# Kernel optimization log

Hardware: AMD Instinct MI355X
Metric: run time of the kernel (lower is better)

Reference implementation:

```python
import jax, jax.numpy as jnp
import numpy as np

HID, OUT = 128, 16
N_USER, N_MOVIE, N_DIR = 200000, 100000, 20000
ALPHA, NUM_LAYERS = 0.01, 2


def _seg_mean(h_src, src, dst, n_dst):
    # copy_u + mean reduce: mean of incoming messages per dst node (0 if no in-edges)
    msg = h_src[src]                                   # [E, H] gather
    s = jax.ops.segment_sum(msg, dst, num_segments=n_dst)
    deg = jax.ops.segment_sum(jnp.ones((dst.shape[0],), h_src.dtype), dst, num_segments=n_dst)
    return s / jnp.maximum(deg, 1.0)[:, None]


def setup_inputs() -> dict:
    key = jax.random.key(0)
    ks = jax.random.split(key, 16)
    inp = {
        'x_user': jax.random.normal(ks[0], (N_USER, 128), jnp.float32),
        'x_movie': jax.random.normal(ks[1], (N_MOVIE, 128), jnp.float32),
        'x_director': jax.random.normal(ks[2], (N_DIR, 128), jnp.float32),
        'rates_src': jax.random.randint(ks[3], (600000,), 0, N_USER, jnp.int32),
        'rates_dst': jax.random.randint(ks[4], (600000,), 0, N_MOVIE, jnp.int32),
        'rby_src': jax.random.randint(ks[5], (600000,), 0, N_MOVIE, jnp.int32),
        'rby_dst': jax.random.randint(ks[6], (600000,), 0, N_USER, jnp.int32),
        'dir_src': jax.random.randint(ks[7], (100000,), 0, N_DIR, jnp.int32),
        'dir_dst': jax.random.randint(ks[8], (100000,), 0, N_MOVIE, jnp.int32),
        'dby_src': jax.random.randint(ks[9], (100000,), 0, N_MOVIE, jnp.int32),
        'dby_dst': jax.random.randint(ks[10], (100000,), 0, N_DIR, jnp.int32),
    }
    sc = 1.0 / np.sqrt(128.0)
    inp['W_user'] = jax.random.normal(ks[11], (HID, 128), jnp.float32) * sc
    inp['b_user'] = jnp.zeros((HID,), jnp.float32)
    inp['W_movie'] = jax.random.normal(ks[12], (HID, 128), jnp.float32) * sc
    inp['b_movie'] = jnp.zeros((HID,), jnp.float32)
    inp['W_director'] = jax.random.normal(ks[13], (HID, 128), jnp.float32) * sc
    inp['b_director'] = jnp.zeros((HID,), jnp.float32)
    inp['W_out'] = jax.random.normal(ks[14], (OUT, HID), jnp.float32) * (1.0 / np.sqrt(HID))
    inp['b_out'] = jnp.zeros((OUT,), jnp.float32)
    return inp


def reference(x_user, x_movie, x_director,
              W_user, b_user, W_movie, b_movie, W_director, b_director,
              W_out, b_out,
              rates_src, rates_dst, rby_src, rby_dst,
              dir_src, dir_dst, dby_src, dby_dst):
    # per-ntype input Linear + ReLU (num_lins = 1)
    h_u = jax.nn.relu(x_user @ W_user.T + b_user)
    h_m = jax.nn.relu(x_movie @ W_movie.T + b_movie)
    h_d = jax.nn.relu(x_director @ W_director.T + b_director)
    for _ in range(NUM_LAYERS):
        # per-etype segment-mean; cross_reducer='mean' over etypes targeting each ntype
        agg_m = 0.5 * (_seg_mean(h_u, rates_src, rates_dst, N_MOVIE)
                       + _seg_mean(h_d, dir_src, dir_dst, N_MOVIE))
        agg_u = _seg_mean(h_m, rby_src, rby_dst, N_USER)
        agg_d = _seg_mean(h_m, dby_src, dby_dst, N_DIR)
        h_u = ALPHA * h_u + agg_u
        h_m = ALPHA * h_m + agg_m
        h_d = ALPHA * h_d + agg_d
    return h_m @ W_out.T + b_out  # target ntype 'movie' logits [N_MOVIE, OUT]
```

## Files before the change

### kernel.cpp

```cpp
#include <hip/hip_runtime.h>

#define ALPHA 0.01f
#define BIN_SHIFT 10
#define SBIN 1024
#define CAPB 8192

typedef __attribute__((ext_vector_type(8))) short short8v;
typedef __attribute__((ext_vector_type(4))) float float4v;

__device__ __forceinline__ void bsplit(float x, unsigned short& hi, unsigned short& lo) {
  unsigned u = __float_as_uint(x);
  hi = (unsigned short)(u >> 16);
  float r = x - __uint_as_float(u & 0xFFFF0000u);
  lo = (unsigned short)(__float_as_uint(r) >> 16);
}

__device__ __forceinline__ void frag_from8(const float* v, short8v& hi, short8v& lo) {
#pragma unroll
  for (int e = 0; e < 8; ++e) {
    unsigned short h, l;
    bsplit(v[e], h, l);
    hi[e] = (short)h;
    lo[e] = (short)l;
  }
}

__global__ __launch_bounds__(256, 2) void fused_mfma3_kernel(
    const float* __restrict__ Xu, const float* __restrict__ Xm, const float* __restrict__ Xd,
    const float* __restrict__ Wu, const float* __restrict__ Wm, const float* __restrict__ Wd,
    const float* __restrict__ Bu, const float* __restrict__ Bm, const float* __restrict__ Bd,
    const float* __restrict__ Wo,
    float* __restrict__ Gu, float* __restrict__ Gm, float* __restrict__ Gd,
    int NU, int NM, int ND, int bu, int bm)
{
  __shared__ char smem[65536 + 10368] __attribute__((aligned(16)));
  unsigned short* Whi = (unsigned short*)smem;
  unsigned short* Wlo = (unsigned short*)(smem + 32768);
  unsigned short* WoHi = (unsigned short*)(smem + 65536);
  unsigned short* WoLo = (unsigned short*)(smem + 65536 + 4096);

  const float *X, *W, *B;
  float* G;
  int N, bid, nbk;
  if ((int)blockIdx.x < bu)            { X = Xu; W = Wu; B = Bu; G = Gu; N = NU; bid = blockIdx.x;            nbk = bu; }
  else if ((int)blockIdx.x < bu + bm)  { X = Xm; W = Wm; B = Bm; G = Gm; N = NM; bid = blockIdx.x - bu;       nbk = bm; }
  else                                 { X = Xd; W = Wd; B = Bd; G = Gd; N = ND; bid = blockIdx.x - bu - bm;  nbk = gridDim.x - bu - bm; }

  const int t = threadIdx.x;
  const int wave = t >> 6;
  const int lane = t & 63;
  const int s = lane & 15;
  const int q = lane >> 4;
  float* hbuf = (float*)(smem + 65536 + wave * 2176);

#pragma unroll
  for (int i = 0; i < 32; ++i) {
    int p = i * 256 + t;
    int row = p >> 6, c2 = p & 63;
    float w0 = W[row * 128 + c2 * 2];
    float w1 = W[row * 128 + c2 * 2 + 1];
    unsigned short h0, l0, h1, l1;
    bsplit(w0, h0, l0); bsplit(w1, h1, l1);
    int u32idx = row * 64 + ((((c2 * 4) ^ ((row & 7) << 4))) >> 2);
    ((unsigned*)Whi)[u32idx] = (unsigned)h0 | ((unsigned)h1 << 16);
    ((unsigned*)Wlo)[u32idx] = (unsigned)l0 | ((unsigned)l1 << 16);
  }
#pragma unroll
  for (int i = 0; i < 4; ++i) {
    int p = i * 256 + t;
    int row = p >> 6, c2 = p & 63;
    float w0 = Wo[row * 128 + c2 * 2];
    float w1 = Wo[row * 128 + c2 * 2 + 1];
    unsigned short h0, l0, h1, l1;
    bsplit(w0, h0, l0); bsplit(w1, h1, l1);
    int u32idx = row * 64 + ((((c2 * 4) ^ ((row & 7) << 4))) >> 2);
    ((unsigned*)WoHi)[u32idx] = (unsigned)h0 | ((unsigned)h1 << 16);
    ((unsigned*)WoLo)[u32idx] = (unsigned)l0 | ((unsigned)l1 << 16);
  }
  __syncthreads();

  short8v woh[4], wol[4];
  const int woswz = (s & 7) << 4;
#pragma unroll
  for (int ks = 0; ks < 4; ++ks) {
    int off = s * 256 + ((ks * 64 + q * 16) ^ woswz);
    woh[ks] = *(const short8v*)((char*)WoHi + off);
    wol[ks] = *(const short8v*)((char*)WoLo + off);
  }
  float bv[8];
#pragma unroll
  for (int nt = 0; nt < 8; ++nt) bv[nt] = B[nt * 16 + s];
  __syncthreads();

  const int nchunks = (N + 127) >> 7;
  const int bswz = (s & 7) << 4;

  for (int chunk = bid; chunk < nchunks; chunk += nbk) {
    const int rowbase = chunk * 128 + wave * 32;

    short8v ahi[2][4], alo[2][4];
#pragma unroll
    for (int mt = 0; mt < 2; ++mt) {
      int row = rowbase + mt * 16 + s;
      int crow = row < N ? row : (N - 1);
      const float* xr = X + (size_t)crow * 128;
#pragma unroll
      for (int ks = 0; ks < 4; ++ks) {
        float4 f0 = *(const float4*)(xr + ks * 32 + q * 8);
        float4 f1 = *(const float4*)(xr + ks * 32 + q * 8 + 4);
        float v[8] = {f0.x, f0.y, f0.z, f0.w, f1.x, f1.y, f1.z, f1.w};
        frag_from8(v, ahi[mt][ks], alo[mt][ks]);
      }
    }

    float4v acc[2][8];
#pragma unroll
    for (int mt = 0; mt < 2; ++mt)
#pragma unroll
      for (int nt = 0; nt < 8; ++nt) acc[mt][nt] = (float4v){0.f, 0.f, 0.f, 0.f};

#pragma unroll
    for (int ks = 0; ks < 4; ++ks) {
      short8v bh[8];
#pragma unroll
      for (int nt = 0; nt < 8; ++nt) {
        int c = nt * 16 + s;
        int off = c * 256 + ((ks * 64 + q * 16) ^ bswz);
        bh[nt] = *(const short8v*)((char*)Whi + off);
      }
#pragma unroll
      for (int nt = 0; nt < 8; ++nt) {
#pragma unroll
        for (int mt = 0; mt < 2; ++mt) {
          acc[mt][nt] = __builtin_amdgcn_mfma_f32_16x16x32_bf16(ahi[mt][ks], bh[nt], acc[mt][nt], 0, 0, 0);
          acc[mt][nt] = __builtin_amdgcn_mfma_f32_16x16x32_bf16(alo[mt][ks], bh[nt], acc[mt][nt], 0, 0, 0);
        }
      }
#pragma unroll
      for (int nt = 0; nt < 8; ++nt) {
        int c = nt * 16 + s;
        int off = c * 256 + ((ks * 64 + q * 16) ^ bswz);
        short8v bl = *(const short8v*)((char*)Wlo + off);
#pragma unroll
        for (int mt = 0; mt < 2; ++mt)
          acc[mt][nt] = __builtin_amdgcn_mfma_f32_16x16x32_bf16(ahi[mt][ks], bl, acc[mt][nt], 0, 0, 0);
      }
    }

#pragma unroll
    for (int mt = 0; mt < 2; ++mt) {
      float4v gacc = (float4v){0.f, 0.f, 0.f, 0.f};
#pragma unroll
      for (int ks = 0; ks < 4; ++ks) {
#pragma unroll
        for (int j = 0; j < 2; ++j) {
          int nt = 2 * ks + j;
          int cl = j * 16 + s;
#pragma unroll
          for (int e = 0; e < 4; ++e)
            hbuf[cl * 17 + q * 4 + e] = fmaxf(acc[mt][nt][e] + bv[nt], 0.f);
        }
        float hv[8];
#pragma unroll
        for (int e = 0; e < 8; ++e) hv[e] = hbuf[(q * 8 + e) * 17 + s];
        short8v hh, hl;
        frag_from8(hv, hh, hl);
        gacc = __builtin_amdgcn_mfma_f32_16x16x32_bf16(hh, woh[ks], gacc, 0, 0, 0);
        gacc = __builtin_amdgcn_mfma_f32_16x16x32_bf16(hl, woh[ks], gacc, 0, 0, 0);
        gacc = __builtin_amdgcn_mfma_f32_16x16x32_bf16(hh, wol[ks], gacc, 0, 0, 0);
      }
      int grow = rowbase + mt * 16 + 4 * q;
#pragma unroll
      for (int e = 0; e < 4; ++e)
        if (grow + e < N) G[(size_t)(grow + e) * 16 + s] = gacc[e];
    }
  }
}

__device__ __forceinline__ void edge_decode(
    int i, const int* ys, const int* yd, int Erby,
    const int* bs, const int* bd, int Edby,
    const int* rs, const int* rd, int Er,
    const int* ds, const int* dd,
    int NU, int& src, int& bucket, int& bin)
{
  if (i < Erby)            { src = ys[i]; bucket = yd[i];                 bin = bucket >> BIN_SHIFT; }
  else if (i < Erby + Edby){ int j = i - Erby; src = bs[j]; bucket = NU + bd[j]; bin = bucket >> BIN_SHIFT; }
  else if (i < Erby + Edby + Er) { int j = i - Erby - Edby; src = rs[j]; bucket = 2 * rd[j]; bin = 256 + (bucket >> BIN_SHIFT); }
  else                     { int j = i - Erby - Edby - Er; src = ds[j]; bucket = 2 * dd[j] + 1; bin = 256 + (bucket >> BIN_SHIFT); }
}

__global__ __launch_bounds__(256) void fill2_kernel(
    const int* __restrict__ ys, const int* __restrict__ yd, int Erby,
    const int* __restrict__ bs, const int* __restrict__ bd, int Edby,
    const int* __restrict__ rs, const int* __restrict__ rd, int Er,
    const int* __restrict__ ds, const int* __restrict__ dd, int Edir,
    int NU, int* __restrict__ cursor,
    unsigned* __restrict__ binnedA, unsigned* __restrict__ binnedB)
{
  __shared__ int h[512];
  __shared__ int base[512];
  const int E = Erby + Edby + Er + Edir;
  const int c0 = blockIdx.x * 4096;
  const int c1 = (c0 + 4096 < E) ? c0 + 4096 : E;
  h[threadIdx.x] = 0; h[threadIdx.x + 256] = 0;
  __syncthreads();
  for (int i = c0 + threadIdx.x; i < c1; i += 256) {
    int src, bucket, bin;
    edge_decode(i, ys, yd, Erby, bs, bd, Edby, rs, rd, Er, ds, dd, NU, src, bucket, bin);
    atomicAdd(&h[bin], 1);
  }
  __syncthreads();
#pragma unroll
  for (int k = threadIdx.x; k < 512; k += 256) {
    int c = h[k];
    base[k] = c ? atomicAdd(&cursor[k], c) : 0;
    h[k] = 0;
  }
  __syncthreads();
  for (int i = c0 + threadIdx.x; i < c1; i += 256) {
    int src, bucket, bin;
    edge_decode(i, ys, yd, Erby, bs, bd, Edby, rs, rd, Er, ds, dd, NU, src, bucket, bin);
    int r = atomicAdd(&h[bin], 1);
    int pos = base[bin] + r;
    if (pos < CAPB) {
      unsigned code = ((unsigned)src << BIN_SHIFT) | (unsigned)(bucket & (SBIN - 1));
      if (bin < 256) binnedA[(size_t)bin * CAPB + pos] = code;
      else           binnedB[(size_t)(bin - 256) * CAPB + pos] = code;
    }
  }
}

__global__ __launch_bounds__(256) void scatter2_kernel(
    const unsigned* __restrict__ binnedA, const unsigned* __restrict__ binnedB,
    const int* __restrict__ cursor, int nbinsA, int HA, int HB,
    int* __restrict__ bOffsA, int* __restrict__ bCntA,
    int* __restrict__ bOffsB, int* __restrict__ bCntB,
    int* __restrict__ ssrcA, int* __restrict__ ssrcB)
{
  __shared__ int cnt[SBIN];
  __shared__ int pref[SBIN];
  __shared__ int wsum[256];
  const int t = threadIdx.x;
  const bool isA = (int)blockIdx.x < nbinsA;
  const int b = isA ? (int)blockIdx.x : (int)blockIdx.x - nbinsA;
  const unsigned* win = (isA ? binnedA : binnedB) + (size_t)b * CAPB;
  int* bOffs = isA ? bOffsA : bOffsB;
  int* bCnt  = isA ? bCntA  : bCntB;
  int* ssrc  = isA ? ssrcA  : ssrcB;
  const int nbuckets = isA ? HA : HB;
  const size_t wbase = (size_t)b * CAPB;
  int n = cursor[isA ? b : 256 + b];
  if (n > CAPB) n = CAPB;

#pragma unroll
  for (int k = t; k < SBIN; k += 256) cnt[k] = 0;
  __syncthreads();
  for (int i = t; i < n; i += 256)
    atomicAdd(&cnt[win[i] & (SBIN - 1)], 1);
  __syncthreads();
  int c0 = cnt[4 * t], c1 = cnt[4 * t + 1], c2 = cnt[4 * t + 2], c3 = cnt[4 * t + 3];
  int s = c0 + c1 + c2 + c3;
  wsum[t] = s;
  __syncthreads();
  for (int d = 1; d < 256; d <<= 1) {
    int add = (t >= d) ? wsum[t - d] : 0;
    __syncthreads();
    wsum[t] += add;
    __syncthreads();
  }
  int base = wsum[t] - s;
  pref[4 * t]     = base;
  pref[4 * t + 1] = base + c0;
  pref[4 * t + 2] = base + c0 + c1;
  pref[4 * t + 3] = base + c0 + c1 + c2;
  __syncthreads();
  const int gb = b << BIN_SHIFT;
#pragma unroll
  for (int k = t; k < SBIN; k += 256) {
    int bucket = gb + k;
    if (bucket < nbuckets) { bOffs[bucket] = (int)(wbase + pref[k]); bCnt[bucket] = cnt[k]; }
  }
  __syncthreads();
#pragma unroll
  for (int k = t; k < SBIN; k += 256) cnt[k] = pref[k];
  __syncthreads();
  for (int i = t; i < n; i += 256) {
    unsigned code = win[i];
    int local = code & (SBIN - 1);
    int r = atomicAdd(&cnt[local], 1);
    ssrc[wbase + r] = (int)(code >> BIN_SHIFT);
  }
}

__global__ __launch_bounds__(256) void gather_pay2_kernel(
    const float* __restrict__ g_m, const float* __restrict__ g_u,
    const float* __restrict__ g_d,
    const int* __restrict__ bOffsA, const int* __restrict__ bCntA,
    const int* __restrict__ ssrcA,
    float* __restrict__ pay_u, float* __restrict__ pay_d, int NU, int ND)
{
  int tid = blockIdx.x * 256 + threadIdx.x;
  int node = tid >> 4, o = tid & 15;
  if (node >= NU + ND) return;
  int start = bOffsA[node], cnt = bCntA[node];
  float sum = 0.f;
  for (int j = 0; j < cnt; ++j) {
    int s = ssrcA[start + j];
    sum += g_m[(size_t)s * 16 + o];
  }
  float mean = 0.5f * sum / fmaxf((float)cnt, 1.f);
  if (node < NU)
    pay_u[(size_t)node * 16 + o] = ALPHA * g_u[(size_t)node * 16 + o] + mean;
  else {
    int nn = node - NU;
    pay_d[(size_t)nn * 16 + o] = ALPHA * g_d[(size_t)nn * 16 + o] + mean;
  }
}

__global__ __launch_bounds__(256) void final_kernel(
    const float* __restrict__ gm, const float* __restrict__ pay_u,
    const float* __restrict__ pay_d,
    const int* __restrict__ bOffs, const int* __restrict__ bCnt,
    const int* __restrict__ ssrc,
    const float* __restrict__ bo, float* __restrict__ out, int NM)
{
  int tid = blockIdx.x * 256 + threadIdx.x;
  int m = tid >> 4, o = tid & 15;
  if (m >= NM) return;
  int s0 = bOffs[2 * m], c0 = bCnt[2 * m];
  float sr = 0.f;
  for (int j = 0; j < c0; ++j) sr += pay_u[(size_t)ssrc[s0 + j] * 16 + o];
  int s1 = bOffs[2 * m + 1], c1 = bCnt[2 * m + 1];
  float sd = 0.f;
  for (int j = 0; j < c1; ++j) sd += pay_d[(size_t)ssrc[s1 + j] * 16 + o];
  out[(size_t)m * 16 + o] = bo[o] + ALPHA * ALPHA * gm[(size_t)m * 16 + o]
                          + sr / fmaxf((float)c0, 1.f) + sd / fmaxf((float)c1, 1.f);
}

extern "C" void kernel_launch(void* const* d_in, const int* in_sizes, int n_in,
                              void* d_out, int out_size, void* d_ws, size_t ws_size,
                              hipStream_t stream)
{
  const float* x_user  = (const float*)d_in[0];
  const float* x_movie = (const float*)d_in[1];
  const float* x_dir   = (const float*)d_in[2];
  const int* rates_src = (const int*)d_in[3];
  const int* rates_dst = (const int*)d_in[4];
  const int* rby_src   = (const int*)d_in[5];
  const int* rby_dst   = (const int*)d_in[6];
  const int* dir_src   = (const int*)d_in[7];
  const int* dir_dst   = (const int*)d_in[8];
  const int* dby_src   = (const int*)d_in[9];
  const int* dby_dst   = (const int*)d_in[10];
  const float* W_user  = (const float*)d_in[11];
  const float* b_user  = (const float*)d_in[12];
  const float* W_movie = (const float*)d_in[13];
  const float* b_movie = (const float*)d_in[14];
  const float* W_dir   = (const float*)d_in[15];
  const float* b_dir   = (const float*)d_in[16];
  const float* W_out   = (const float*)d_in[17];
  const float* b_out   = (const float*)d_in[18];

  const int NU = in_sizes[0] / 128, NM = in_sizes[1] / 128, ND = in_sizes[2] / 128;
  const int Er = in_sizes[3], Erby = in_sizes[5], Edir = in_sizes[7], Edby = in_sizes[9];

  const int E  = Er + Edir + Erby + Edby;
  const int HA = NU + ND;
  const int HB = 2 * NM;
  const int nbinsA = (HA + SBIN - 1) >> BIN_SHIFT;
  const int nbinsB = (HB + SBIN - 1) >> BIN_SHIFT;

  char* w = (char*)d_ws;
  size_t off = 0;
  auto take = [&](size_t bytes) { char* p = w + off; off += (bytes + 255) & ~(size_t)255; return p; };
  float* g_u   = (float*)take((size_t)NU * 16 * 4);
  float* g_m   = (float*)take((size_t)NM * 16 * 4);
  float* g_d   = (float*)take((size_t)ND * 16 * 4);
  float* pay_u = (float*)take((size_t)NU * 16 * 4);
  float* pay_d = (float*)take((size_t)ND * 16 * 4);
  int* cursor     = (int*)take(512 * 4);
  int* bOffsA     = (int*)take((size_t)HA * 4);
  int* bCntA      = (int*)take((size_t)HA * 4);
  int* bOffsB     = (int*)take((size_t)HB * 4);
  int* bCntB      = (int*)take((size_t)HB * 4);
  unsigned* binnedA = (unsigned*)take((size_t)nbinsA * CAPB * 4);
  unsigned* binnedB = (unsigned*)take((size_t)nbinsB * CAPB * 4);
  int* ssrcA      = (int*)take((size_t)nbinsA * CAPB * 4);
  int* ssrcB      = (int*)take((size_t)nbinsB * CAPB * 4);
  if (off > ws_size) return;

  hipMemsetAsync(cursor, 0, 512 * 4, stream);

  fill2_kernel<<<(E + 4095) / 4096, 256, 0, stream>>>(
      rby_src, rby_dst, Erby, dby_src, dby_dst, Edby,
      rates_src, rates_dst, Er, dir_src, dir_dst, Edir, NU,
      cursor, binnedA, binnedB);

  scatter2_kernel<<<nbinsA + nbinsB, 256, 0, stream>>>(
      binnedA, binnedB, cursor, nbinsA, HA, HB,
      bOffsA, bCntA, bOffsB, bCntB, ssrcA, ssrcB);

  {
    long long cu = (NU + 127) >> 7, cm = (NM + 127) >> 7, cd = (ND + 127) >> 7;
    long long ct = cu + cm + cd;
    int bu = (int)((512 * cu + ct / 2) / ct);
    int bm = (int)((512 * cm + ct / 2) / ct);
    if (bu < 1) bu = 1;
    if (bm < 1) bm = 1;
    if (bu + bm > 510) { bu = 510 * bu / (bu + bm); bm = 510 - bu; }
    fused_mfma3_kernel<<<512, 256, 0, stream>>>(
        x_user, x_movie, x_dir, W_user, W_movie, W_dir,
        b_user, b_movie, b_dir, W_out, g_u, g_m, g_d,
        NU, NM, ND, bu, bm);
  }

  gather_pay2_kernel<<<((NU + ND) * 16 + 255) / 256, 256, 0, stream>>>(
      g_m, g_u, g_d, bOffsA, bCntA, ssrcA, pay_u, pay_d, NU, ND);

  final_kernel<<<(NM * 16 + 255) / 256, 256, 0, stream>>>(
      g_m, pay_u, pay_d, bOffsB, bCntB, ssrcB, b_out, (float*)d_out, NM);
}
```

Measured before the change: 159.9 us.

## Transpose MFMA operands to skip LDS round-trip in the output projection

```diff
diff --git a/kernel.cpp b/kernel.cpp
--- a/kernel.cpp
+++ b/kernel.cpp
@@ -33,11 +33,12 @@
     float* __restrict__ Gu, float* __restrict__ Gm, float* __restrict__ Gd,
     int NU, int NM, int ND, int bu, int bm)
 {
-  __shared__ char smem[65536 + 10368] __attribute__((aligned(16)));
+  __shared__ char smem[65536 + 8192 + 512] __attribute__((aligned(16)));
   unsigned short* Whi = (unsigned short*)smem;
   unsigned short* Wlo = (unsigned short*)(smem + 32768);
   unsigned short* WoHi = (unsigned short*)(smem + 65536);
   unsigned short* WoLo = (unsigned short*)(smem + 65536 + 4096);
+  float* Bs = (float*)(smem + 65536 + 8192);
 
   const float *X, *W, *B;
   float* G;
@@ -51,7 +52,6 @@
   const int lane = t & 63;
   const int s = lane & 15;
   const int q = lane >> 4;
-  float* hbuf = (float*)(smem + 65536 + wave * 2176);
 
 #pragma unroll
   for (int i = 0; i < 32; ++i) {
@@ -69,31 +69,25 @@
   for (int i = 0; i < 4; ++i) {
     int p = i * 256 + t;
     int row = p >> 6, c2 = p & 63;
-    float w0 = Wo[row * 128 + c2 * 2];
-    float w1 = Wo[row * 128 + c2 * 2 + 1];
+    int kp = 2 * c2;
+    int j = kp >> 5;
+    int t5 = kp & 31;
+    int qq = t5 >> 3, e = t5 & 7;
+    int c0 = 32 * j + (e < 4 ? 4 * qq + e : 16 + 4 * qq + (e - 4));
+    float w0 = Wo[row * 128 + c0];
+    float w1 = Wo[row * 128 + c0 + 1];
     unsigned short h0, l0, h1, l1;
     bsplit(w0, h0, l0); bsplit(w1, h1, l1);
     int u32idx = row * 64 + ((((c2 * 4) ^ ((row & 7) << 4))) >> 2);
     ((unsigned*)WoHi)[u32idx] = (unsigned)h0 | ((unsigned)h1 << 16);
     ((unsigned*)WoLo)[u32idx] = (unsigned)l0 | ((unsigned)l1 << 16);
   }
-  __syncthreads();
-
-  short8v woh[4], wol[4];
-  const int woswz = (s & 7) << 4;
-#pragma unroll
-  for (int ks = 0; ks < 4; ++ks) {
-    int off = s * 256 + ((ks * 64 + q * 16) ^ woswz);
-    woh[ks] = *(const short8v*)((char*)WoHi + off);
-    wol[ks] = *(const short8v*)((char*)WoLo + off);
-  }
-  float bv[8];
-#pragma unroll
-  for (int nt = 0; nt < 8; ++nt) bv[nt] = B[nt * 16 + s];
+  if (t < 32) ((float4*)Bs)[t] = ((const float4*)B)[t];
   __syncthreads();
 
   const int nchunks = (N + 127) >> 7;
   const int bswz = (s & 7) << 4;
+  const int woswz = (s & 7) << 4;
 
   for (int chunk = bid; chunk < nchunks; chunk += nbk) {
     const int rowbase = chunk * 128 + wave * 32;
@@ -132,8 +126,8 @@
       for (int nt = 0; nt < 8; ++nt) {
 #pragma unroll
         for (int mt = 0; mt < 2; ++mt) {
-          acc[mt][nt] = __builtin_amdgcn_mfma_f32_16x16x32_bf16(ahi[mt][ks], bh[nt], acc[mt][nt], 0, 0, 0);
-          acc[mt][nt] = __builtin_amdgcn_mfma_f32_16x16x32_bf16(alo[mt][ks], bh[nt], acc[mt][nt], 0, 0, 0);
+          acc[mt][nt] = __builtin_amdgcn_mfma_f32_16x16x32_bf16(bh[nt], ahi[mt][ks], acc[mt][nt], 0, 0, 0);
+          acc[mt][nt] = __builtin_amdgcn_mfma_f32_16x16x32_bf16(bh[nt], alo[mt][ks], acc[mt][nt], 0, 0, 0);
         }
       }
 #pragma unroll
@@ -143,36 +137,44 @@
         short8v bl = *(const short8v*)((char*)Wlo + off);
 #pragma unroll
         for (int mt = 0; mt < 2; ++mt)
-          acc[mt][nt] = __builtin_amdgcn_mfma_f32_16x16x32_bf16(ahi[mt][ks], bl, acc[mt][nt], 0, 0, 0);
+          acc[mt][nt] = __builtin_amdgcn_mfma_f32_16x16x32_bf16(bl, ahi[mt][ks], acc[mt][nt], 0, 0, 0);
       }
     }
 
-#pragma unroll
-    for (int mt = 0; mt < 2; ++mt) {
-      float4v gacc = (float4v){0.f, 0.f, 0.f, 0.f};
-#pragma unroll
-      for (int ks = 0; ks < 4; ++ks) {
-#pragma unroll
-        for (int j = 0; j < 2; ++j) {
-          int nt = 2 * ks + j;
-          int cl = j * 16 + s;
-#pragma unroll
-          for (int e = 0; e < 4; ++e)
-            hbuf[cl * 17 + q * 4 + e] = fmaxf(acc[mt][nt][e] + bv[nt], 0.f);
-        }
+    float4v gacc[2];
+    gacc[0] = (float4v){0.f, 0.f, 0.f, 0.f};
+    gacc[1] = (float4v){0.f, 0.f, 0.f, 0.f};
+#pragma unroll
+    for (int j = 0; j < 4; ++j) {
+      int off = s * 256 + ((j * 64 + q * 16) ^ woswz);
+      short8v wohj = *(const short8v*)((char*)WoHi + off);
+      short8v wolj = *(const short8v*)((char*)WoLo + off);
+      float4 b4a = *(const float4*)(Bs + 32 * j + 4 * q);
+      float4 b4b = *(const float4*)(Bs + 32 * j + 16 + 4 * q);
+#pragma unroll
+      for (int mt = 0; mt < 2; ++mt) {
         float hv[8];
-#pragma unroll
-        for (int e = 0; e < 8; ++e) hv[e] = hbuf[(q * 8 + e) * 17 + s];
+        hv[0] = fmaxf(acc[mt][2 * j][0] + b4a.x, 0.f);
+        hv[1] = fmaxf(acc[mt][2 * j][1] + b4a.y, 0.f);
+        hv[2] = fmaxf(acc[mt][2 * j][2] + b4a.z, 0.f);
+        hv[3] = fmaxf(acc[mt][2 * j][3] + b4a.w, 0.f);
+        hv[4] = fmaxf(acc[mt][2 * j + 1][0] + b4b.x, 0.f);
+        hv[5] = fmaxf(acc[mt][2 * j + 1][1] + b4b.y, 0.f);
+        hv[6] = fmaxf(acc[mt][2 * j + 1][2] + b4b.z, 0.f);
+        hv[7] = fmaxf(acc[mt][2 * j + 1][3] + b4b.w, 0.f);
         short8v hh, hl;
         frag_from8(hv, hh, hl);
-        gacc = __builtin_amdgcn_mfma_f32_16x16x32_bf16(hh, woh[ks], gacc, 0, 0, 0);
-        gacc = __builtin_amdgcn_mfma_f32_16x16x32_bf16(hl, woh[ks], gacc, 0, 0, 0);
-        gacc = __builtin_amdgcn_mfma_f32_16x16x32_bf16(hh, wol[ks], gacc, 0, 0, 0);
+        gacc[mt] = __builtin_amdgcn_mfma_f32_16x16x32_bf16(wohj, hh, gacc[mt], 0, 0, 0);
+        gacc[mt] = __builtin_amdgcn_mfma_f32_16x16x32_bf16(wohj, hl, gacc[mt], 0, 0, 0);
+        gacc[mt] = __builtin_amdgcn_mfma_f32_16x16x32_bf16(wolj, hh, gacc[mt], 0, 0, 0);
       }
-      int grow = rowbase + mt * 16 + 4 * q;
-#pragma unroll
-      for (int e = 0; e < 4; ++e)
-        if (grow + e < N) G[(size_t)(grow + e) * 16 + s] = gacc[e];
+    }
+#pragma unroll
+    for (int mt = 0; mt < 2; ++mt) {
+      int grow = rowbase + mt * 16 + s;
+      if (grow < N)
+        *(float4*)(G + (size_t)grow * 16 + 4 * q) =
+            make_float4(gacc[mt][0], gacc[mt][1], gacc[mt][2], gacc[mt][3]);
     }
   }
 }
```

Measured after the change: 253.9 us. 58.8% more time.
